# Kernel optimization log

Measured on AMD Instinct MI355X. Metric: run time of the kernel, lower is better.

## Reference

```python
import math
import jax, jax.numpy as jnp
import numpy as np

N_HEAD = 8
D_QKV = 8192
D_HEAD = D_QKV // N_HEAD  # 1024


def setup_inputs() -> dict:
    k0 = jax.random.key(0)
    k1, k2, k3 = jax.random.split(k0, 3)
    return {
        "query": jax.random.normal(k1, (256, 2048, 256), dtype=jnp.float32),
        "key": jax.random.normal(k2, (256, 64, 256), dtype=jnp.float32),
        "value": jax.random.normal(k3, (512, 256, 4), dtype=jnp.float32),
    }


def reference(query, key, value):
    # n_state = last dim of key (fixing the original's key.size() bug),
    # bsz = key.size(1), per the torch forward.
    n_state = key.shape[-1]  # 256
    bsz = key.shape[1]       # 64
    # (d0, Lq, n_state) @ (d0, n_state, bsz) -> (d0, Lq, bsz)
    v1 = jnp.matmul(query, jnp.swapaxes(key, -2, -1)) / math.sqrt(n_state)
    # reshape to (X, bsz*n_head, n_state), transpose(0,1), softmax over dim 1
    aw = jax.nn.softmax(
        jnp.swapaxes(v1.reshape(-1, bsz * N_HEAD, n_state), 0, 1), axis=1
    )  # (bsz*n_head, X, n_state)
    # (bsz*n_head, X, n_state) @ (bsz*n_head, n_state, d_v) -> (bsz*n_head, X, d_v)
    out = jnp.matmul(aw.reshape(bsz * N_HEAD, -1, n_state), value)
    return out.reshape(bsz, N_HEAD, D_HEAD)
```

## Files before the change

### kernel.cpp

```cpp
#include <hip/hip_runtime.h>
#include <hip/hip_bf16.h>


typedef __attribute__((ext_vector_type(8))) short bf16x8;
typedef __attribute__((ext_vector_type(4))) float floatx4;

__device__ inline short bf16bits(float f) {
    union { __hip_bfloat16 h; short s; } u;
    u.h = __float2bfloat16(f);
    return u.s;
}

__device__ inline bf16x8 load_cvt8(const float* p) {
    float4 f0 = *reinterpret_cast<const float4*>(p);
    float4 f1 = *reinterpret_cast<const float4*>(p + 4);
    bf16x8 r;
    r[0] = bf16bits(f0.x); r[1] = bf16bits(f0.y);
    r[2] = bf16bits(f0.z); r[3] = bf16bits(f0.w);
    r[4] = bf16bits(f1.x); r[5] = bf16bits(f1.y);
    r[6] = bf16bits(f1.z); r[7] = bf16bits(f1.w);
    return r;
}

__global__ __launch_bounds__(256) void qkt_exp_kernel(
    const float* __restrict__ q,
    const float* __restrict__ k,
    __hip_bfloat16* __restrict__ expS)
{
    __shared__ __hip_bfloat16 ksh[64 * 264];

    const int x     = blockIdx.y;
    const int ltile = blockIdx.x;
    const int t     = threadIdx.x;
    const int wave  = t >> 6;
    const int lane  = t & 63;
    const int lrow  = lane & 15;
    const int kgrp  = lane >> 4;

    const float* kbase = k + (size_t)x * 64 * 256;
#pragma unroll
    for (int j = 0; j < 16; j++) {
        int e = j * 1024 + t * 4;
        float4 f = *reinterpret_cast<const float4*>(kbase + e);
        int row = e >> 8, col = e & 255;
        __hip_bfloat16* d = &ksh[row * 264 + col];
        union { __hip_bfloat16 h; short s; } u;
        u.s = bf16bits(f.x); d[0] = u.h;
        u.s = bf16bits(f.y); d[1] = u.h;
        u.s = bf16bits(f.z); d[2] = u.h;
        u.s = bf16bits(f.w); d[3] = u.h;
    }
    __syncthreads();

    const float* qbase =
        q + ((size_t)x * 2048 + (size_t)(ltile * 128 + wave * 32)) * 256;

    floatx4 acc[2][4];
#pragma unroll
    for (int i = 0; i < 2; i++)
#pragma unroll
        for (int j = 0; j < 4; j++) acc[i][j] = (floatx4)0.f;

#pragma unroll
    for (int k0 = 0; k0 < 256; k0 += 32) {
        bf16x8 a[2], b[4];
#pragma unroll
        for (int mt = 0; mt < 2; mt++)
            a[mt] = load_cvt8(qbase + (size_t)(mt * 16 + lrow) * 256 + k0 + kgrp * 8);
#pragma unroll
        for (int nt = 0; nt < 4; nt++)
            b[nt] = *reinterpret_cast<const bf16x8*>(
                &ksh[(nt * 16 + lrow) * 264 + k0 + kgrp * 8]);
#pragma unroll
        for (int mt = 0; mt < 2; mt++)
#pragma unroll
            for (int nt = 0; nt < 4; nt++)
                acc[mt][nt] = __builtin_amdgcn_mfma_f32_16x16x32_bf16(
                    a[mt], b[nt], acc[mt][nt], 0, 0, 0);
    }

    __hip_bfloat16* sbase =
        expS + (size_t)x * 131072 + (size_t)(ltile * 128 + wave * 32) * 64;
    const int col   = lane & 15;
    const int rbase = (lane >> 4) * 4;
#pragma unroll
    for (int mt = 0; mt < 2; mt++)
#pragma unroll
        for (int nt = 0; nt < 4; nt++)
#pragma unroll
            for (int r = 0; r < 4; r++) {
                float p = __expf(acc[mt][nt][r] * 0.0625f);
                sbase[(size_t)(mt * 16 + rbase + r) * 64 + nt * 16 + col] =
                    __float2bfloat16(p);
            }
}

__global__ __launch_bounds__(256) void colsum_kernel(
    const __hip_bfloat16* __restrict__ expS,
    float* __restrict__ rl)
{
    const int r = blockIdx.x * 256 + threadIdx.x;
    const __hip_bfloat16* p = expS + r;
    float s = 0.f;
#pragma unroll 8
    for (int x = 0; x < 256; x++)
        s += __bfloat162float(p[(size_t)x * 131072]);
    rl[r] = 1.f / s;
}

__global__ __launch_bounds__(256) void out_kernel(
    const __hip_bfloat16* __restrict__ expS,
    const float* __restrict__ rl,
    const float* __restrict__ v,
    float* __restrict__ out)
{
    __shared__ __hip_bfloat16 tile[256 * 66];
    __shared__ float vs[64][4];

    const int y = blockIdx.x;
    const int t = threadIdx.x;

    float acc0 = 0.f, acc1 = 0.f, acc2 = 0.f, acc3 = 0.f;

    for (int zc = 0; zc < 256; zc += 64) {
        {
            const int z  = t & 63;
            const int xw = t >> 6;
            const __hip_bfloat16* gp = expS + (size_t)y * 256 + zc + z;
#pragma unroll 8
            for (int i = 0; i < 64; i++) {
                int xx = i * 4 + xw;
                tile[xx * 66 + z] = gp[(size_t)xx * 131072];
            }
        }
        if (t < 64) {
            int r = y * 256 + zc + t;
            float rlv = rl[r];
            float4 vv = *reinterpret_cast<const float4*>(v + (size_t)r * 4);
            vs[t][0] = vv.x * rlv;
            vs[t][1] = vv.y * rlv;
            vs[t][2] = vv.z * rlv;
            vs[t][3] = vv.w * rlv;
        }
        __syncthreads();

#pragma unroll 8
        for (int z = 0; z < 64; z++) {
            float p = __bfloat162float(tile[t * 66 + z]);
            acc0 += p * vs[z][0];
            acc1 += p * vs[z][1];
            acc2 += p * vs[z][2];
            acc3 += p * vs[z][3];
        }
        __syncthreads();
    }

    float4 o = make_float4(acc0, acc1, acc2, acc3);
    *reinterpret_cast<float4*>(out + ((size_t)y * 256 + t) * 4) = o;
}

extern "C" void kernel_launch(void* const* d_in, const int* in_sizes, int n_in,
                              void* d_out, int out_size, void* d_ws, size_t ws_size,
                              hipStream_t stream) {
    const float* q = (const float*)d_in[0];
    const float* k = (const float*)d_in[1];
    const float* v = (const float*)d_in[2];
    float* out = (float*)d_out;

    __hip_bfloat16* expS = (__hip_bfloat16*)d_ws;
    float* rl = (float*)((char*)d_ws + 67108864);

    qkt_exp_kernel<<<dim3(16, 256), 256, 0, stream>>>(q, k, expS);
    colsum_kernel<<<dim3(512), 256, 0, stream>>>(expS, rl);
    out_kernel<<<dim3(512), 256, 0, stream>>>(expS, rl, v, out);
}
```

Measured before the change: 754.8 us.

## Fuse column-sum normalization into output kernel and vectorize K smem stores

Removes the separate colsum kernel. The softmax denominators are now computed inside out_kernel while it already loads each expS tile, with partial sums reduced through shared memory. This saves a full strided pass over the 64MB expS buffer and one kernel launch, at the cost of an extra barrier per chunk. It also packs the bf16 conversions of K into single short4 shared-memory stores.

```diff
diff --git a/kernel.cpp b/kernel.cpp
--- a/kernel.cpp
+++ b/kernel.cpp
@@ -43,12 +43,12 @@
         int e = j * 1024 + t * 4;
         float4 f = *reinterpret_cast<const float4*>(kbase + e);
         int row = e >> 8, col = e & 255;
-        __hip_bfloat16* d = &ksh[row * 264 + col];
-        union { __hip_bfloat16 h; short s; } u;
-        u.s = bf16bits(f.x); d[0] = u.h;
-        u.s = bf16bits(f.y); d[1] = u.h;
-        u.s = bf16bits(f.z); d[2] = u.h;
-        u.s = bf16bits(f.w); d[3] = u.h;
+        short4 sv;
+        sv.x = bf16bits(f.x);
+        sv.y = bf16bits(f.y);
+        sv.z = bf16bits(f.z);
+        sv.w = bf16bits(f.w);
+        *reinterpret_cast<short4*>(&ksh[row * 264 + col]) = sv;
     }
     __syncthreads();
 
@@ -95,47 +95,41 @@
             }
 }
 
-__global__ __launch_bounds__(256) void colsum_kernel(
-    const __hip_bfloat16* __restrict__ expS,
-    float* __restrict__ rl)
-{
-    const int r = blockIdx.x * 256 + threadIdx.x;
-    const __hip_bfloat16* p = expS + r;
-    float s = 0.f;
-#pragma unroll 8
-    for (int x = 0; x < 256; x++)
-        s += __bfloat162float(p[(size_t)x * 131072]);
-    rl[r] = 1.f / s;
-}
-
 __global__ __launch_bounds__(256) void out_kernel(
     const __hip_bfloat16* __restrict__ expS,
-    const float* __restrict__ rl,
     const float* __restrict__ v,
     float* __restrict__ out)
 {
     __shared__ __hip_bfloat16 tile[256 * 66];
+    __shared__ float psum[64][4];
     __shared__ float vs[64][4];
 
-    const int y = blockIdx.x;
-    const int t = threadIdx.x;
+    const int y  = blockIdx.x;
+    const int t  = threadIdx.x;
+    const int z  = t & 63;
+    const int xw = t >> 6;
 
     float acc0 = 0.f, acc1 = 0.f, acc2 = 0.f, acc3 = 0.f;
 
     for (int zc = 0; zc < 256; zc += 64) {
         {
-            const int z  = t & 63;
-            const int xw = t >> 6;
             const __hip_bfloat16* gp = expS + (size_t)y * 256 + zc + z;
-#pragma unroll 8
+            float ls = 0.f;
+#pragma unroll 16
             for (int i = 0; i < 64; i++) {
                 int xx = i * 4 + xw;
-                tile[xx * 66 + z] = gp[(size_t)xx * 131072];
+                __hip_bfloat16 bv = gp[(size_t)xx * 131072];
+                tile[xx * 66 + z] = bv;
+                ls += __bfloat162float(bv);
             }
+            psum[z][xw] = ls;
         }
+        __syncthreads();
+
         if (t < 64) {
+            float s = psum[t][0] + psum[t][1] + psum[t][2] + psum[t][3];
+            float rlv = 1.f / s;
             int r = y * 256 + zc + t;
-            float rlv = rl[r];
             float4 vv = *reinterpret_cast<const float4*>(v + (size_t)r * 4);
             vs[t][0] = vv.x * rlv;
             vs[t][1] = vv.y * rlv;
@@ -145,12 +139,12 @@
         __syncthreads();
 
 #pragma unroll 8
-        for (int z = 0; z < 64; z++) {
-            float p = __bfloat162float(tile[t * 66 + z]);
-            acc0 += p * vs[z][0];
-            acc1 += p * vs[z][1];
-            acc2 += p * vs[z][2];
-            acc3 += p * vs[z][3];
+        for (int zz = 0; zz < 64; zz++) {
+            float p = __bfloat162float(tile[t * 66 + zz]);
+            acc0 += p * vs[zz][0];
+            acc1 += p * vs[zz][1];
+            acc2 += p * vs[zz][2];
+            acc3 += p * vs[zz][3];
         }
         __syncthreads();
     }
@@ -168,9 +162,7 @@
     float* out = (float*)d_out;
 
     __hip_bfloat16* expS = (__hip_bfloat16*)d_ws;
-    float* rl = (float*)((char*)d_ws + 67108864);
 
     qkt_exp_kernel<<<dim3(16, 256), 256, 0, stream>>>(q, k, expS);
-    colsum_kernel<<<dim3(512), 256, 0, stream>>>(expS, rl);
-    out_kernel<<<dim3(512), 256, 0, stream>>>(expS, rl, v, out);
+    out_kernel<<<dim3(512), 256, 0, stream>>>(expS, v, out);
 }
```

Measured after the change: 733.8 us. 2.8% less time.
